# Kernel tuning notes

Measured on AMD Instinct MI355X. Metric: run time of the kernel, lower is better.

## Reference

```python
import jax, jax.numpy as jnp
import numpy as np

D = 256
NUM_STAB = 1024
NUM_CYCLES = 128
B, S = 64, 4096
EPS = 1e-5


def setup_inputs() -> dict:
    key = jax.random.key(0)
    ks = jax.random.split(key, 32)
    inp = {
        'meas': jax.random.normal(ks[0], (B, S), jnp.float32),
        'event': jax.random.normal(ks[1], (B, S), jnp.float32),
        'leak': jax.random.uniform(ks[2], (B, S), jnp.float32),
        'event_leak': jax.random.uniform(ks[3], (B, S), jnp.float32),
        'stab_ids': jax.random.randint(ks[4], (B, S), 0, NUM_STAB),
        'cycle_ids': jax.random.randint(ks[5], (B, S), 0, NUM_CYCLES),
        # Linear(1, d): weight is a length-d vector, plus bias
        'w_meas': jax.random.normal(ks[6], (D,), jnp.float32) * 0.02,
        'b_meas': jnp.zeros((D,), jnp.float32),
        'w_event': jax.random.normal(ks[7], (D,), jnp.float32) * 0.02,
        'b_event': jnp.zeros((D,), jnp.float32),
        'w_leak': jax.random.normal(ks[8], (D,), jnp.float32) * 0.02,
        'b_leak': jnp.zeros((D,), jnp.float32),
        'w_el': jax.random.normal(ks[9], (D,), jnp.float32) * 0.02,
        'b_el': jnp.zeros((D,), jnp.float32),
        'stab_table': jax.random.normal(ks[10], (NUM_STAB, D), jnp.float32) * 0.02,
        'cycle_table': jax.random.normal(ks[11], (NUM_CYCLES, D), jnp.float32) * 0.02,
        # res block 1
        'g1': jnp.ones((D,), jnp.float32),
        'be1': jnp.zeros((D,), jnp.float32),
        'W11': jax.random.normal(ks[12], (D, D), jnp.float32) * (1.0 / np.sqrt(D)),
        'b11': jnp.zeros((D,), jnp.float32),
        'W12': jax.random.normal(ks[13], (D, D), jnp.float32) * (1.0 / np.sqrt(D)),
        'b12': jnp.zeros((D,), jnp.float32),
        # res block 2
        'g2': jnp.ones((D,), jnp.float32),
        'be2': jnp.zeros((D,), jnp.float32),
        'W21': jax.random.normal(ks[14], (D, D), jnp.float32) * (1.0 / np.sqrt(D)),
        'b21': jnp.zeros((D,), jnp.float32),
        'W22': jax.random.normal(ks[15], (D, D), jnp.float32) * (1.0 / np.sqrt(D)),
        'b22': jnp.zeros((D,), jnp.float32),
    }
    return inp


def _layernorm(x, g, b):
    mu = jnp.mean(x, axis=-1, keepdims=True)
    var = jnp.mean(jnp.square(x - mu), axis=-1, keepdims=True)
    return (x - mu) * jax.lax.rsqrt(var + EPS) * g + b


def _res_block(x, g, be, W1, b1, W2, b2):
    h = _layernorm(x, g, be)
    h = jax.nn.gelu(h @ W1 + b1, approximate=False)  # torch F.gelu default = exact erf
    return x + h @ W2 + b2


def reference(meas, event, leak, event_leak, stab_ids, cycle_ids,
              w_meas, b_meas, w_event, b_event, w_leak, b_leak, w_el, b_el,
              stab_table, cycle_table,
              g1, be1, W11, b11, W12, b12,
              g2, be2, W21, b21, W22, b22):
    # Linear(1,d)(x.unsqueeze(-1)) == x[...,None]*w + b; fuse the four projections.
    h = (meas[..., None] * w_meas + b_meas
         + event[..., None] * w_event + b_event
         + leak[..., None] * w_leak + b_leak
         + event_leak[..., None] * w_el + b_el
         + stab_table[stab_ids]
         + cycle_table[cycle_ids])  # (B, S, D)
    h = _res_block(h, g1, be1, W11, b11, W12, b12)
    h = _res_block(h, g2, be2, W21, b21, W22, b22)
    return h
```

## Files before the change

kernel.cpp:

```cpp
#include <hip/hip_runtime.h>

#define NTOK 262144
#define TT 64
#define EPS 1e-5f

typedef short short8 __attribute__((ext_vector_type(8)));
typedef float float4v __attribute__((ext_vector_type(4)));

__device__ __align__(16) short g_Wp[4 * 65536];

__device__ __forceinline__ short f2bf(float f) {
    uint32_t u = __builtin_bit_cast(uint32_t, f);
    u += 0x7FFFu + ((u >> 16) & 1u);
    return (short)(u >> 16);
}

__global__ void pack_w(const float* __restrict__ W11, const float* __restrict__ W12,
                       const float* __restrict__ W21, const float* __restrict__ W22) {
    int t = blockIdx.x * 256 + threadIdx.x;
    int g = t >> 16;
    int r = t & 65535;
    int j = r & 7, l = (r >> 3) & 63, kb = (r >> 9) & 7, nt = (r >> 12) & 15;
    int n = nt * 16 + (l & 15);
    int k = kb * 32 + (l >> 4) * 8 + j;
    const float* W = (g == 0) ? W11 : (g == 1) ? W12 : (g == 2) ? W21 : W22;
    g_Wp[t] = f2bf(W[k * 256 + n]);
}

__device__ __forceinline__ float gelu_erf(float v) {
    float z = fabsf(v) * 0.70710678118654752f;
    float d = __builtin_fmaf(0.3275911f, z, 1.0f);
    float t;
    asm("v_rcp_f32 %0, %1" : "=v"(t) : "v"(d));
    float poly = t * (0.254829592f + t * (-0.284496736f + t * (1.421413741f
               + t * (-1.453152027f + t * 1.061405429f))));
    float er = 1.0f - poly * __expf(-z * z);
    er = copysignf(er, v);
    return 0.5f * v * (1.0f + er);
}

__device__ __forceinline__ int aidx(int m, int k) {
    int lp = (m & 15) | (((k >> 3) & 3) << 4);
    int gs = (lp >> 2) | ((lp & 3) << 4);
    return ((((m >> 4) * 8 + (k >> 5)) * 64) + gs) * 8 + (k & 7);
}

__global__ __launch_bounds__(512, 1) void fused_kernel(
    const float* __restrict__ meas, const float* __restrict__ event,
    const float* __restrict__ leak, const float* __restrict__ elk,
    const int* __restrict__ sids, const int* __restrict__ cids,
    const float* __restrict__ w_meas, const float* __restrict__ w_event,
    const float* __restrict__ w_leak, const float* __restrict__ w_el,
    const float* __restrict__ b_meas, const float* __restrict__ b_event,
    const float* __restrict__ b_leak, const float* __restrict__ b_el,
    const float* __restrict__ stab_table, const float* __restrict__ cycle_table,
    const float* __restrict__ g1, const float* __restrict__ be1,
    const float* __restrict__ b11, const float* __restrict__ b12,
    const float* __restrict__ g2, const float* __restrict__ be2,
    const float* __restrict__ b21, const float* __restrict__ b22,
    float* __restrict__ out)
{
    __shared__ __align__(16) short Abuf[2][4 * 8 * 64 * 8];
    __shared__ float par[8 * 256];
    __shared__ __align__(16) float ubuf[2][768];

    const int tid = threadIdx.x;
    const int w = tid >> 6;
    const int half = w >> 2;
    const int wh = w & 3;
    const int lane = tid & 63;
    const int q = lane >> 4, c = lane & 15;
    const int gl = (lane >> 2) | ((lane & 3) << 4);
    const int R0h = blockIdx.x * 2 * TT + half * TT;

    float (*rowf)[TT] = (float (*)[TT])ubuf[half];
    int   (*rowi)[TT] = (int (*)[TT])(ubuf[half] + 256);
    float *redp = ubuf[half];
    short *Ah = Abuf[half];

    float wm[4], we[4], wl[4], w2[4], bs[4];
    #pragma unroll
    for (int ntl = 0; ntl < 4; ++ntl) {
        int n = wh * 64 + ntl * 16 + c;
        wm[ntl] = w_meas[n];
        we[ntl] = w_event[n];
        wl[ntl] = w_leak[n];
        w2[ntl] = w_el[n];
        bs[ntl] = b_meas[n] + b_event[n] + b_leak[n] + b_el[n];
    }

    if (tid < 256) {
        int n = tid;
        par[0 * 256 + n] = g1[n];
        par[1 * 256 + n] = be1[n];
        par[2 * 256 + n] = b11[n];
        par[3 * 256 + n] = b12[n];
        par[4 * 256 + n] = g2[n];
        par[5 * 256 + n] = be2[n];
        par[6 * 256 + n] = b21[n];
        par[7 * 256 + n] = b22[n];
    }
    {
        int th = tid & 255;
        if (th < TT) {
            rowf[0][th] = meas[R0h + th];
            rowf[1][th] = event[R0h + th];
            rowf[2][th] = leak[R0h + th];
            rowf[3][th] = elk[R0h + th];
            rowi[0][th] = sids[R0h + th];
            rowi[1][th] = cids[R0h + th];
        }
    }
    __syncthreads();

    float xr[4][4][4];
    #pragma unroll
    for (int rg = 0; rg < 4; ++rg)
        #pragma unroll
        for (int reg = 0; reg < 4; ++reg) {
            int m = rg * 16 + 4 * q + reg;
            float mv = rowf[0][m], ev = rowf[1][m], lv = rowf[2][m], e2 = rowf[3][m];
            const float* srow = stab_table + rowi[0][m] * 256;
            const float* crow = cycle_table + rowi[1][m] * 256;
            #pragma unroll
            for (int ntl = 0; ntl < 4; ++ntl) {
                int n = wh * 64 + ntl * 16 + c;
                xr[rg][ntl][reg] = mv * wm[ntl] + ev * we[ntl] + lv * wl[ntl]
                                 + e2 * w2[ntl] + bs[ntl] + srow[n] + crow[n];
            }
        }
    __syncthreads();

    float4v acc[4][4];

    auto ln_reduce = [&]() {
        float s[4][4], s2[4][4];
        #pragma unroll
        for (int rg = 0; rg < 4; ++rg)
            #pragma unroll
            for (int reg = 0; reg < 4; ++reg) {
                float a = 0.f, b = 0.f;
                #pragma unroll
                for (int ntl = 0; ntl < 4; ++ntl) {
                    float v = xr[rg][ntl][reg];
                    a += v; b += v * v;
                }
                #pragma unroll
                for (int d = 1; d < 16; d <<= 1) {
                    a += __shfl_xor(a, d, 64);
                    b += __shfl_xor(b, d, 64);
                }
                s[rg][reg] = a; s2[rg][reg] = b;
            }
        if (c == 0) {
            #pragma unroll
            for (int rg = 0; rg < 4; ++rg)
                #pragma unroll
                for (int reg = 0; reg < 4; ++reg) {
                    int m = rg * 16 + 4 * q + reg;
                    redp[m * 12 + wh] = s[rg][reg];
                    redp[m * 12 + 4 + wh] = s2[rg][reg];
                }
        }
    };

    auto ln_write = [&](const float* g, const float* be) {
        float gv[4], bv[4];
        #pragma unroll
        for (int ntl = 0; ntl < 4; ++ntl) {
            int n = wh * 64 + ntl * 16 + c;
            gv[ntl] = g[n]; bv[ntl] = be[n];
        }
        #pragma unroll
        for (int rg = 0; rg < 4; ++rg)
            #pragma unroll
            for (int reg = 0; reg < 4; ++reg) {
                int m = rg * 16 + 4 * q + reg;
                float4v a4 = *(const float4v*)&redp[m * 12];
                float4v b4 = *(const float4v*)&redp[m * 12 + 4];
                float a = a4[0] + a4[1] + a4[2] + a4[3];
                float b = b4[0] + b4[1] + b4[2] + b4[3];
                float mu = a * (1.0f / 256.0f);
                float ve = b * (1.0f / 256.0f) - mu * mu + EPS;
                float rs;
                asm("v_rsq_f32 %0, %1" : "=v"(rs) : "v"(ve));
                #pragma unroll
                for (int ntl = 0; ntl < 4; ++ntl) {
                    int n = wh * 64 + ntl * 16 + c;
                    Ah[aidx(m, n)] = f2bf((xr[rg][ntl][reg] - mu) * rs * gv[ntl] + bv[ntl]);
                }
            }
    };

    short8 bh0[4];
    auto preB = [&](int g4) {
        const short* W = g_Wp + g4 * 65536;
        #pragma unroll
        for (int ntl = 0; ntl < 4; ++ntl) {
            int nt = wh * 4 + ntl;
            bh0[ntl] = *(const short8*)&W[((nt * 8 + 0) * 64 + lane) * 8];
        }
    };

    auto do_gemm = [&](int g4) {
        const short* W = g_Wp + g4 * 65536;
        #pragma unroll
        for (int rg = 0; rg < 4; ++rg)
            #pragma unroll
            for (int ntl = 0; ntl < 4; ++ntl)
                acc[rg][ntl] = (float4v){0.f, 0.f, 0.f, 0.f};
        short8 ah[2][4], bh[2][4];
        #pragma unroll
        for (int rg = 0; rg < 4; ++rg)
            ah[0][rg] = *(const short8*)&Ah[((rg * 8 + 0) * 64 + gl) * 8];
        #pragma unroll
        for (int ntl = 0; ntl < 4; ++ntl)
            bh[0][ntl] = bh0[ntl];
        #pragma unroll
        for (int kb = 0; kb < 8; ++kb) {
            const int cur = kb & 1, nxt = cur ^ 1;
            if (kb < 7) {
                #pragma unroll
                for (int rg = 0; rg < 4; ++rg)
                    ah[nxt][rg] = *(const short8*)&Ah[((rg * 8 + kb + 1) * 64 + gl) * 8];
                #pragma unroll
                for (int ntl = 0; ntl < 4; ++ntl) {
                    int nt = wh * 4 + ntl;
                    bh[nxt][ntl] = *(const short8*)&W[((nt * 8 + kb + 1) * 64 + lane) * 8];
                }
            }
            __builtin_amdgcn_s_setprio(1);
            #pragma unroll
            for (int rg = 0; rg < 4; ++rg)
                #pragma unroll
                for (int ntl = 0; ntl < 4; ++ntl)
                    acc[rg][ntl] = __builtin_amdgcn_mfma_f32_16x16x32_bf16(
                        ah[cur][rg], bh[cur][ntl], acc[rg][ntl], 0, 0, 0);
            __builtin_amdgcn_s_setprio(0);
        }
    };

    auto gelu_write = [&](const float* bias) {
        float bv[4];
        #pragma unroll
        for (int ntl = 0; ntl < 4; ++ntl)
            bv[ntl] = bias[wh * 64 + ntl * 16 + c];
        #pragma unroll
        for (int rg = 0; rg < 4; ++rg)
            #pragma unroll
            for (int ntl = 0; ntl < 4; ++ntl)
                #pragma unroll
                for (int reg = 0; reg < 4; ++reg) {
                    int m = rg * 16 + 4 * q + reg;
                    int n = wh * 64 + ntl * 16 + c;
                    Ah[aidx(m, n)] = f2bf(gelu_erf(acc[rg][ntl][reg] + bv[ntl]));
                }
    };

    auto resadd = [&]() {
        float bv[4];
        #pragma unroll
        for (int ntl = 0; ntl < 4; ++ntl)
            bv[ntl] = par[3 * 256 + wh * 64 + ntl * 16 + c];
        #pragma unroll
        for (int rg = 0; rg < 4; ++rg)
            #pragma unroll
            for (int ntl = 0; ntl < 4; ++ntl)
                #pragma unroll
                for (int reg = 0; reg < 4; ++reg)
                    xr[rg][ntl][reg] += acc[rg][ntl][reg] + bv[ntl];
    };

    auto store_out = [&]() {
        float bv[4];
        #pragma unroll
        for (int ntl = 0; ntl < 4; ++ntl)
            bv[ntl] = par[7 * 256 + wh * 64 + ntl * 16 + c];
        #pragma unroll
        for (int rg = 0; rg < 4; ++rg)
            #pragma unroll
            for (int ntl = 0; ntl < 4; ++ntl)
                #pragma unroll
                for (int reg = 0; reg < 4; ++reg) {
                    int m = rg * 16 + 4 * q + reg;
                    int n = wh * 64 + ntl * 16 + c;
                    out[(size_t)(R0h + m) * 256 + n] =
                        xr[rg][ntl][reg] + acc[rg][ntl][reg] + bv[ntl];
                }
    };

    if (!half) ln_reduce();
    __syncthreads();
    if (!half) { preB(0); ln_write(par + 0 * 256, par + 1 * 256); } else ln_reduce();
    __syncthreads();
    if (!half) do_gemm(0); else { preB(0); ln_write(par + 0 * 256, par + 1 * 256); }
    __syncthreads();
    if (!half) { preB(1); gelu_write(par + 2 * 256); } else do_gemm(0);
    __syncthreads();
    if (!half) do_gemm(1); else { preB(1); gelu_write(par + 2 * 256); }
    __syncthreads();
    if (!half) resadd(); else do_gemm(1);
    __syncthreads();
    if (!half) ln_reduce(); else resadd();
    __syncthreads();
    if (!half) { preB(2); ln_write(par + 4 * 256, par + 5 * 256); } else ln_reduce();
    __syncthreads();
    if (!half) do_gemm(2); else { preB(2); ln_write(par + 4 * 256, par + 5 * 256); }
    __syncthreads();
    if (!half) { preB(3); gelu_write(par + 6 * 256); } else do_gemm(2);
    __syncthreads();
    if (!half) do_gemm(3); else { preB(3); gelu_write(par + 6 * 256); }
    __syncthreads();
    if (!half) store_out(); else do_gemm(3);
    if (half) store_out();
}

extern "C" void kernel_launch(void* const* d_in, const int* in_sizes, int n_in,
                              void* d_out, int out_size, void* d_ws, size_t ws_size,
                              hipStream_t stream) {
    pack_w<<<1024, 256, 0, stream>>>(
        (const float*)d_in[18], (const float*)d_in[20],
        (const float*)d_in[24], (const float*)d_in[26]);
    fused_kernel<<<NTOK / (2 * TT), 512, 0, stream>>>(
        (const float*)d_in[0], (const float*)d_in[1],
        (const float*)d_in[2], (const float*)d_in[3],
        (const int*)d_in[4], (const int*)d_in[5],
        (const float*)d_in[6], (const float*)d_in[8],
        (const float*)d_in[10], (const float*)d_in[12],
        (const float*)d_in[7], (const float*)d_in[9],
        (const float*)d_in[11], (const float*)d_in[13],
        (const float*)d_in[14], (const float*)d_in[15],
        (const float*)d_in[16], (const float*)d_in[17],
        (const float*)d_in[19], (const float*)d_in[21],
        (const float*)d_in[22], (const float*)d_in[23],
        (const float*)d_in[25], (const float*)d_in[27],
        (float*)d_out);
}
```

Baseline: 612.7 us.

## Fold LayerNorm into first GEMM via precomputed gamma·W and beta·W+bias

Rewrites LN(x)@W1+b1 as rs*(x*g)@W1 - rs*mu*(g@W1) + (be@W1+b1), with the two vectors computed by a small prep kernel. The GEMM A operand is then written right away as bf16(x*g), and the row statistics are reduced in the same pass, so the separate ln_reduce phase and two barriers per block go away. Mean and rstd are applied in the GELU epilogue. Cancellation risk increases because mu*gW is subtracted from a bf16-accumulated product, and the raw x is quantized to bf16 instead of the normalized value.

```diff
diff --git a/kernel.cpp b/kernel.cpp
--- a/kernel.cpp
+++ b/kernel.cpp
@@ -8,6 +8,7 @@
 typedef float float4v __attribute__((ext_vector_type(4)));
 
 __device__ __align__(16) short g_Wp[4 * 65536];
+__device__ float g_par[4 * 256];
 
 __device__ __forceinline__ short f2bf(float f) {
     uint32_t u = __builtin_bit_cast(uint32_t, f);
@@ -25,6 +26,20 @@
     int k = kb * 32 + (l >> 4) * 8 + j;
     const float* W = (g == 0) ? W11 : (g == 1) ? W12 : (g == 2) ? W21 : W22;
     g_Wp[t] = f2bf(W[k * 256 + n]);
+}
+
+__global__ void prep_par(const float* __restrict__ g1, const float* __restrict__ be1,
+                         const float* __restrict__ b11, const float* __restrict__ W11,
+                         const float* __restrict__ g2, const float* __restrict__ be2,
+                         const float* __restrict__ b21, const float* __restrict__ W21) {
+    int j = threadIdx.x, l = blockIdx.x;
+    const float* W = (l < 2) ? W11 : W21;
+    const float* v = (l == 0) ? g1 : (l == 1) ? be1 : (l == 2) ? g2 : be2;
+    float s = 0.f;
+    for (int n = 0; n < 256; ++n) s = __builtin_fmaf(v[n], W[n * 256 + j], s);
+    if (l == 1) s += b11[j];
+    if (l == 3) s += b21[j];
+    g_par[l * 256 + j] = s;
 }
 
 __device__ __forceinline__ float gelu_erf(float v) {
@@ -62,7 +77,7 @@
 {
     __shared__ __align__(16) short Abuf[2][4 * 8 * 64 * 8];
     __shared__ float par[8 * 256];
-    __shared__ __align__(16) float ubuf[2][768];
+    __shared__ __align__(16) float ubuf[2][1152];
 
     const int tid = threadIdx.x;
     const int w = tid >> 6;
@@ -75,7 +90,7 @@
 
     float (*rowf)[TT] = (float (*)[TT])ubuf[half];
     int   (*rowi)[TT] = (int (*)[TT])(ubuf[half] + 256);
-    float *redp = ubuf[half];
+    float *redp = ubuf[half] + 384;
     short *Ah = Abuf[half];
 
     float wm[4], we[4], wl[4], w2[4], bs[4];
@@ -92,12 +107,12 @@
     if (tid < 256) {
         int n = tid;
         par[0 * 256 + n] = g1[n];
-        par[1 * 256 + n] = be1[n];
-        par[2 * 256 + n] = b11[n];
+        par[1 * 256 + n] = g_par[0 * 256 + n];
+        par[2 * 256 + n] = g_par[1 * 256 + n];
         par[3 * 256 + n] = b12[n];
         par[4 * 256 + n] = g2[n];
-        par[5 * 256 + n] = be2[n];
-        par[6 * 256 + n] = b21[n];
+        par[5 * 256 + n] = g_par[2 * 256 + n];
+        par[6 * 256 + n] = g_par[3 * 256 + n];
         par[7 * 256 + n] = b22[n];
     }
     {
@@ -129,12 +144,25 @@
                                  + e2 * w2[ntl] + bs[ntl] + srow[n] + crow[n];
             }
         }
-    __syncthreads();
 
     float4v acc[4][4];
 
-    auto ln_reduce = [&]() {
-        float s[4][4], s2[4][4];
+    auto aw_write = [&](const float* g) {
+        float gv[4];
+        #pragma unroll
+        for (int ntl = 0; ntl < 4; ++ntl)
+            gv[ntl] = g[wh * 64 + ntl * 16 + c];
+        #pragma unroll
+        for (int rg = 0; rg < 4; ++rg)
+            #pragma unroll
+            for (int reg = 0; reg < 4; ++reg) {
+                int m = rg * 16 + 4 * q + reg;
+                #pragma unroll
+                for (int ntl = 0; ntl < 4; ++ntl) {
+                    int n = wh * 64 + ntl * 16 + c;
+                    Ah[aidx(m, n)] = f2bf(xr[rg][ntl][reg] * gv[ntl]);
+                }
+            }
         #pragma unroll
         for (int rg = 0; rg < 4; ++rg)
             #pragma unroll
@@ -150,26 +178,20 @@
                     a += __shfl_xor(a, d, 64);
                     b += __shfl_xor(b, d, 64);
                 }
-                s[rg][reg] = a; s2[rg][reg] = b;
-            }
-        if (c == 0) {
-            #pragma unroll
-            for (int rg = 0; rg < 4; ++rg)
-                #pragma unroll
-                for (int reg = 0; reg < 4; ++reg) {
+                if (c == 0) {
                     int m = rg * 16 + 4 * q + reg;
-                    redp[m * 12 + wh] = s[rg][reg];
-                    redp[m * 12 + 4 + wh] = s2[rg][reg];
-                }
-        }
-    };
-
-    auto ln_write = [&](const float* g, const float* be) {
-        float gv[4], bv[4];
+                    redp[m * 12 + wh] = a;
+                    redp[m * 12 + 4 + wh] = b;
+                }
+            }
+    };
+
+    auto u_write = [&](const float* gw, const float* bw) {
+        float gwv[4], bwv[4];
         #pragma unroll
         for (int ntl = 0; ntl < 4; ++ntl) {
             int n = wh * 64 + ntl * 16 + c;
-            gv[ntl] = g[n]; bv[ntl] = be[n];
+            gwv[ntl] = gw[n]; bwv[ntl] = bw[n];
         }
         #pragma unroll
         for (int rg = 0; rg < 4; ++rg)
@@ -187,7 +209,8 @@
                 #pragma unroll
                 for (int ntl = 0; ntl < 4; ++ntl) {
                     int n = wh * 64 + ntl * 16 + c;
-                    Ah[aidx(m, n)] = f2bf((xr[rg][ntl][reg] - mu) * rs * gv[ntl] + bv[ntl]);
+                    float h = rs * (acc[rg][ntl][reg] - mu * gwv[ntl]) + bwv[ntl];
+                    Ah[aidx(m, n)] = f2bf(gelu_erf(h));
                 }
             }
     };
@@ -238,23 +261,6 @@
                         ah[cur][rg], bh[cur][ntl], acc[rg][ntl], 0, 0, 0);
             __builtin_amdgcn_s_setprio(0);
         }
-    };
-
-    auto gelu_write = [&](const float* bias) {
-        float bv[4];
-        #pragma unroll
-        for (int ntl = 0; ntl < 4; ++ntl)
-            bv[ntl] = bias[wh * 64 + ntl * 16 + c];
-        #pragma unroll
-        for (int rg = 0; rg < 4; ++rg)
-            #pragma unroll
-            for (int ntl = 0; ntl < 4; ++ntl)
-                #pragma unroll
-                for (int reg = 0; reg < 4; ++reg) {
-                    int m = rg * 16 + 4 * q + reg;
-                    int n = wh * 64 + ntl * 16 + c;
-                    Ah[aidx(m, n)] = f2bf(gelu_erf(acc[rg][ntl][reg] + bv[ntl]));
-                }
     };
 
     auto resadd = [&]() {
@@ -289,27 +295,21 @@
                 }
     };
 
-    if (!half) ln_reduce();
-    __syncthreads();
-    if (!half) { preB(0); ln_write(par + 0 * 256, par + 1 * 256); } else ln_reduce();
-    __syncthreads();
-    if (!half) do_gemm(0); else { preB(0); ln_write(par + 0 * 256, par + 1 * 256); }
-    __syncthreads();
-    if (!half) { preB(1); gelu_write(par + 2 * 256); } else do_gemm(0);
-    __syncthreads();
-    if (!half) do_gemm(1); else { preB(1); gelu_write(par + 2 * 256); }
-    __syncthreads();
-    if (!half) resadd(); else do_gemm(1);
-    __syncthreads();
-    if (!half) ln_reduce(); else resadd();
-    __syncthreads();
-    if (!half) { preB(2); ln_write(par + 4 * 256, par + 5 * 256); } else ln_reduce();
-    __syncthreads();
-    if (!half) do_gemm(2); else { preB(2); ln_write(par + 4 * 256, par + 5 * 256); }
-    __syncthreads();
-    if (!half) { preB(3); gelu_write(par + 6 * 256); } else do_gemm(2);
-    __syncthreads();
-    if (!half) do_gemm(3); else { preB(3); gelu_write(par + 6 * 256); }
+    if (!half) { preB(0); aw_write(par + 0 * 256); }
+    __syncthreads();
+    if (!half) do_gemm(0); else { preB(0); aw_write(par + 0 * 256); }
+    __syncthreads();
+    if (!half) { preB(1); u_write(par + 1 * 256, par + 2 * 256); } else do_gemm(0);
+    __syncthreads();
+    if (!half) do_gemm(1); else { preB(1); u_write(par + 1 * 256, par + 2 * 256); }
+    __syncthreads();
+    if (!half) { preB(2); resadd(); aw_write(par + 4 * 256); } else do_gemm(1);
+    __syncthreads();
+    if (!half) do_gemm(2); else { preB(2); resadd(); aw_write(par + 4 * 256); }
+    __syncthreads();
+    if (!half) { preB(3); u_write(par + 5 * 256, par + 6 * 256); } else do_gemm(2);
+    __syncthreads();
+    if (!half) do_gemm(3); else { preB(3); u_write(par + 5 * 256, par + 6 * 256); }
     __syncthreads();
     if (!half) store_out(); else do_gemm(3);
     if (half) store_out();
@@ -321,6 +321,11 @@
     pack_w<<<1024, 256, 0, stream>>>(
         (const float*)d_in[18], (const float*)d_in[20],
         (const float*)d_in[24], (const float*)d_in[26]);
+    prep_par<<<4, 256, 0, stream>>>(
+        (const float*)d_in[16], (const float*)d_in[17],
+        (const float*)d_in[19], (const float*)d_in[18],
+        (const float*)d_in[22], (const float*)d_in[23],
+        (const float*)d_in[25], (const float*)d_in[24]);
     fused_kernel<<<NTOK / (2 * TT), 512, 0, stream>>>(
         (const float*)d_in[0], (const float*)d_in[1],
         (const float*)d_in[2], (const float*)d_in[3],
```

After: 659.0 us. +7.6%, slower.
